# Performance work log

Measured on AMD Instinct MI355X. Metric: run time of the kernel, lower is better.

Reference implementation:

```python
import jax, jax.numpy as jnp
import numpy as np

N = 1_000_000
D_IN = 57   # hardcoded reshape(1,57) in original aggregate()
D_OUT = 128
K = 3       # num_sample=3 hardcoded in _get_unique_neighs_list


def _masked_mean_aggregate(h, neigh_idx, neigh_mask):
    # h: [N, D]; neigh_idx: [N, K] int; neigh_mask: [N, K] {0,1}
    feats = h[neigh_idx]                                   # [N, K, D] gather
    m = neigh_mask.astype(h.dtype)[..., None]              # [N, K, 1]
    s = jnp.sum(feats * m, axis=1)                         # [N, D]
    cnt = jnp.maximum(jnp.sum(neigh_mask, axis=1, keepdims=True).astype(h.dtype), 1.0)
    return s / cnt                                         # mask.mm(embed_matrix) equivalent (segment mean)


def _sage_layer(self_feats, aggregate_feats, W):
    # combined = cat([self, agg], dim=1); relu(W @ combined^T)^T; L2 normalize
    combined = jnp.concatenate([self_feats, aggregate_feats], axis=1)  # [N, 2D]
    out = jax.nn.relu(combined @ W.T)                                  # [N, out]
    norm = jnp.linalg.norm(out, axis=-1, keepdims=True)
    return out / jnp.maximum(norm, 1e-12)                              # F.normalize p=2 eps=1e-12


def setup_inputs() -> dict:
    key = jax.random.key(0)
    ks = jax.random.split(key, 7)
    x = jax.random.normal(ks[0], (N, D_IN), dtype=jnp.float32)
    W1 = jax.random.normal(ks[1], (D_OUT, 2 * D_IN), dtype=jnp.float32) * 0.1
    W2 = jax.random.normal(ks[2], (D_OUT, 2 * D_OUT), dtype=jnp.float32) * 0.1
    neigh_idx1 = jax.random.randint(ks[3], (N, K), 0, N, dtype=jnp.int32)
    neigh_mask1 = jax.random.randint(ks[4], (N, K), 0, 2, dtype=jnp.int32)
    neigh_idx2 = jax.random.randint(ks[5], (N, K), 0, N, dtype=jnp.int32)
    neigh_mask2 = jax.random.randint(ks[6], (N, K), 0, 2, dtype=jnp.int32)
    return {"x": x, "W1": W1, "W2": W2,
            "neigh_idx1": neigh_idx1, "neigh_mask1": neigh_mask1,
            "neigh_idx2": neigh_idx2, "neigh_mask2": neigh_mask2}


def reference(x, W1, W2, neigh_idx1, neigh_mask1, neigh_idx2, neigh_mask2):
    # Layer 1: aggregate over sampled neighbors of raw features, then SageLayer
    agg1 = _masked_mean_aggregate(x, neigh_idx1, neigh_mask1)
    h1 = _sage_layer(x, agg1, W1)                 # [N, D_OUT]
    # Layer 2
    agg2 = _masked_mean_aggregate(h1, neigh_idx2, neigh_mask2)
    h2 = _sage_layer(h1, agg2, W2)                # [N, D_OUT]
    return h2
```

## Files before the change

### kernel.cpp

```cpp
#include <hip/hip_runtime.h>
#include <hip/hip_bf16.h>

#define NN 1000000
#define NG 15625
#define GRID 512

typedef short bf16x8 __attribute__((ext_vector_type(8)));
typedef float f32x4  __attribute__((ext_vector_type(4)));
typedef unsigned short u16x8 __attribute__((ext_vector_type(8)));
typedef unsigned short u16x4 __attribute__((ext_vector_type(4)));

__device__ __forceinline__ float bf2f(unsigned short u){
  unsigned int x = ((unsigned int)u) << 16; float f;
  __builtin_memcpy(&f, &x, 4); return f;
}
__device__ __forceinline__ short f2bf(float v){
  __hip_bfloat16 h = __float2bfloat16(v); short s;
  __builtin_memcpy(&s, &h, 2); return s;
}

__global__ __launch_bounds__(512, 2) void sage2_mfma(
    const unsigned short* __restrict__ h1, const float* __restrict__ W2,
    const int* __restrict__ nidx, const int* __restrict__ nmask,
    float* __restrict__ out)
{
  __shared__ unsigned short comb[2][64 * 256];
  __shared__ float red[64][8];
  const int t   = threadIdx.x;
  const int l   = t & 63;
  const int w   = t >> 6;
  const int cfr = l & 15;
  const int kg  = l >> 4;

  bf16x8 Bf[8];
  #pragma unroll
  for (int ks = 0; ks < 8; ++ks) {
    const int col = w*16 + cfr;
    const int k0  = ks*32 + kg*8;
    const float* p = W2 + col*256 + k0;
    f32x4 a = *reinterpret_cast<const f32x4*>(p);
    f32x4 b = *reinterpret_cast<const f32x4*>(p + 4);
    bf16x8 v;
    v[0]=f2bf(a[0]); v[1]=f2bf(a[1]); v[2]=f2bf(a[2]); v[3]=f2bf(a[3]);
    v[4]=f2bf(b[0]); v[5]=f2bf(b[1]); v[6]=f2bf(b[2]); v[7]=f2bf(b[3]);
    Bf[ks] = v;
  }

  const u16x8* hp = reinterpret_cast<const u16x8*>(h1);

  int nib0[2], nib1[2], nib2[2], nmb0[2], nmb1[2], nmb2[2];
  u16x8 sS[2], s0[2], s1[2], s2[2];
  float m0[2], m1[2], m2[2], iv[2];

  auto IDX = [&](int g){
    const long gb = (long)g * 64;
    #pragma unroll
    for (int i = 0; i < 2; ++i) {
      int n = (t + i*512) >> 4;
      long node = gb + n;
      nib0[i] = nidx[node*3+0]; nib1[i] = nidx[node*3+1]; nib2[i] = nidx[node*3+2];
      nmb0[i] = nmask[node*3+0]; nmb1[i] = nmask[node*3+1]; nmb2[i] = nmask[node*3+2];
    }
  };
  auto GATHER = [&](int g){
    const long gb = (long)g * 64;
    #pragma unroll
    for (int i = 0; i < 2; ++i) {
      int it = t + i*512;
      int n = it >> 4, q = it & 15;
      long node = gb + n;
      int b0 = nmb0[i], b1 = nmb1[i], b2 = nmb2[i];
      m0[i]=(float)b0; m1[i]=(float)b1; m2[i]=(float)b2;
      int c = b0+b1+b2; iv[i] = 1.0f/(float)(c<1?1:c);
      u16x8 z = {};
      sS[i] = hp[node*16 + q];
      s0[i] = b0 ? hp[(long)nib0[i]*16 + q] : z;
      s1[i] = b1 ? hp[(long)nib1[i]*16 + q] : z;
      s2[i] = b2 ? hp[(long)nib2[i]*16 + q] : z;
    }
  };
  auto UNPACK = [&](int p){
    char* cb = reinterpret_cast<char*>(comb[p]);
    #pragma unroll
    for (int i = 0; i < 2; ++i) {
      int it = t + i*512;
      int n = it >> 4, q = it & 15;
      int sw = (n & 7) << 4;
      *reinterpret_cast<u16x8*>(cb + n*512 + ((q*16) ^ sw)) = sS[i];
      u16x8 r;
      #pragma unroll
      for (int j = 0; j < 8; ++j)
        r[j] = (unsigned short)f2bf(
            (m0[i]*bf2f(s0[i][j]) + m1[i]*bf2f(s1[i][j]) + m2[i]*bf2f(s2[i][j])) * iv[i]);
      *reinterpret_cast<u16x8*>(cb + n*512 + ((256 + q*16) ^ sw)) = r;
    }
  };

  const int g0 = blockIdx.x;
  IDX(g0); GATHER(g0);
  if (g0 + (int)gridDim.x < NG) IDX(g0 + gridDim.x);

  int p = 0;
  for (int g = g0; g < NG; g += gridDim.x) {
    const long gb = (long)g * 64;
    UNPACK(p);
    __syncthreads();

    int g1 = g + gridDim.x, g2 = g + 2*gridDim.x;
    if (g1 < NG) GATHER(g1);
    if (g2 < NG) IDX(g2);

    f32x4 acc[4];
    #pragma unroll
    for (int r = 0; r < 4; ++r) acc[r] = (f32x4){0.f,0.f,0.f,0.f};
    const int swz = (cfr & 7) << 4;
    char* cbp = reinterpret_cast<char*>(comb[p]);
    #pragma unroll
    for (int r = 0; r < 4; ++r) {
      const int rb = (r*16 + cfr) * 512;
      #pragma unroll
      for (int ks = 0; ks < 8; ++ks) {
        bf16x8 af = *reinterpret_cast<const bf16x8*>(cbp + rb + ((ks*64 + kg*16) ^ swz));
        acc[r] = __builtin_amdgcn_mfma_f32_16x16x32_bf16(af, Bf[ks], acc[r], 0,0,0);
      }
    }

    float ssv[4][4];
    #pragma unroll
    for (int r = 0; r < 4; ++r) {
      #pragma unroll
      for (int e = 0; e < 4; ++e) {
        float v = fmaxf(acc[r][e], 0.f); acc[r][e] = v;
        float s = v*v;
        s += __shfl_xor(s, 1); s += __shfl_xor(s, 2);
        s += __shfl_xor(s, 4); s += __shfl_xor(s, 8);
        ssv[r][e] = s;
      }
      if (cfr < 4) {
        float v = cfr==0 ? ssv[r][0] : cfr==1 ? ssv[r][1] : cfr==2 ? ssv[r][2] : ssv[r][3];
        red[r*16 + kg*4 + cfr][w] = v;
      }
    }
    __syncthreads();

    #pragma unroll
    for (int r = 0; r < 4; ++r) {
      #pragma unroll
      for (int e = 0; e < 4; ++e) {
        int row = r*16 + kg*4 + e;
        f32x4 ra = *reinterpret_cast<const f32x4*>(&red[row][0]);
        f32x4 rb = *reinterpret_cast<const f32x4*>(&red[row][4]);
        float tot = (ra[0]+ra[1]) + (ra[2]+ra[3]) + (rb[0]+rb[1]) + (rb[2]+rb[3]);
        float inv = 1.0f / fmaxf(sqrtf(tot), 1e-12f);
        out[(gb + row)*128 + w*16 + cfr] = acc[r][e] * inv;
      }
    }
    p ^= 1;
  }
}

__global__ __launch_bounds__(512, 2) void sage1_mfma(
    const float* __restrict__ x, const float* __restrict__ W1,
    const int* __restrict__ nidx, const int* __restrict__ nmask,
    unsigned short* __restrict__ h1)
{
  __shared__ unsigned short comb[2][64 * 128];
  __shared__ float red[64][8];
  const int t   = threadIdx.x;
  const int l   = t & 63;
  const int w   = t >> 6;
  const int cfr = l & 15;
  const int kg  = l >> 4;

  bf16x8 Bf[4];
  #pragma unroll
  for (int ks = 0; ks < 4; ++ks) {
    const int col = w*16 + cfr;
    const int k0  = ks*32 + kg*8;
    bf16x8 v;
    #pragma unroll
    for (int j = 0; j < 8; ++j) {
      int lk = k0 + j;
      int wk = lk < 64 ? lk : lk - 7;
      bool valid = (lk < 57) || (lk >= 64 && lk < 121);
      v[j] = valid ? f2bf(W1[col*114 + wk]) : (short)0;
    }
    Bf[ks] = v;
  }

  int nib0[2], nib1[2], nib2[2], nmb0[2], nmb1[2], nmb2[2];
  f32x4 sf[2], n0[2], n1[2], n2[2];
  float m0[2], m1[2], m2[2], iv[2];

  auto IDX = [&](int g){
    const long gb = (long)g * 64;
    #pragma unroll
    for (int i = 0; i < 2; ++i) {
      int n = (t + i*512) >> 4;
      long node = gb + n;
      nib0[i] = nidx[node*3+0]; nib1[i] = nidx[node*3+1]; nib2[i] = nidx[node*3+2];
      nmb0[i] = nmask[node*3+0]; nmb1[i] = nmask[node*3+1]; nmb2[i] = nmask[node*3+2];
    }
  };
  auto GATHER = [&](int g){
    const long gb = (long)g * 64;
    #pragma unroll
    for (int i = 0; i < 2; ++i) {
      int it = t + i*512;
      int n = it >> 4, q = it & 15;
      long node = gb + n;
      int b0 = nmb0[i], b1 = nmb1[i], b2 = nmb2[i];
      m0[i]=(float)b0; m1[i]=(float)b1; m2[i]=(float)b2;
      int c = b0+b1+b2; iv[i] = 1.0f/(float)(c<1?1:c);
      #pragma unroll
      for (int jj = 0; jj < 4; ++jj) {
        int j = q*4 + jj; int jc = j < 57 ? j : 56;
        sf[i][jj] = x[node*57 + jc];
        n0[i][jj] = b0 ? x[(long)nib0[i]*57 + jc] : 0.f;
        n1[i][jj] = b1 ? x[(long)nib1[i]*57 + jc] : 0.f;
        n2[i][jj] = b2 ? x[(long)nib2[i]*57 + jc] : 0.f;
      }
    }
  };
  auto UNPACK = [&](int p){
    char* cb = reinterpret_cast<char*>(comb[p]);
    #pragma unroll
    for (int i = 0; i < 2; ++i) {
      int it = t + i*512;
      int n = it >> 4, q = it & 15;
      int sw = (n & 7) << 4;
      u16x4 vs, va;
      #pragma unroll
      for (int jj = 0; jj < 4; ++jj) {
        vs[jj] = (unsigned short)f2bf(sf[i][jj]);
        va[jj] = (unsigned short)f2bf(
            (m0[i]*n0[i][jj] + m1[i]*n1[i][jj] + m2[i]*n2[i][jj]) * iv[i]);
      }
      *reinterpret_cast<u16x4*>(cb + n*256 + ((q*8) ^ sw))       = vs;
      *reinterpret_cast<u16x4*>(cb + n*256 + ((128 + q*8) ^ sw)) = va;
    }
  };

  const int g0 = blockIdx.x;
  IDX(g0); GATHER(g0);
  if (g0 + (int)gridDim.x < NG) IDX(g0 + gridDim.x);

  int p = 0;
  for (int g = g0; g < NG; g += gridDim.x) {
    const long gb = (long)g * 64;
    UNPACK(p);
    __syncthreads();

    int g1 = g + gridDim.x, g2 = g + 2*gridDim.x;
    if (g1 < NG) GATHER(g1);
    if (g2 < NG) IDX(g2);

    f32x4 acc[4];
    #pragma unroll
    for (int r = 0; r < 4; ++r) acc[r] = (f32x4){0.f,0.f,0.f,0.f};
    const int swz = (cfr & 7) << 4;
    char* cbp = reinterpret_cast<char*>(comb[p]);
    #pragma unroll
    for (int r = 0; r < 4; ++r) {
      const int rb = (r*16 + cfr) * 256;
      #pragma unroll
      for (int ks = 0; ks < 4; ++ks) {
        bf16x8 af = *reinterpret_cast<const bf16x8*>(cbp + rb + ((ks*64 + kg*16) ^ swz));
        acc[r] = __builtin_amdgcn_mfma_f32_16x16x32_bf16(af, Bf[ks], acc[r], 0,0,0);
      }
    }

    float ssv[4][4];
    #pragma unroll
    for (int r = 0; r < 4; ++r) {
      #pragma unroll
      for (int e = 0; e < 4; ++e) {
        float v = fmaxf(acc[r][e], 0.f); acc[r][e] = v;
        float s = v*v;
        s += __shfl_xor(s, 1); s += __shfl_xor(s, 2);
        s += __shfl_xor(s, 4); s += __shfl_xor(s, 8);
        ssv[r][e] = s;
      }
      if (cfr < 4) {
        float v = cfr==0 ? ssv[r][0] : cfr==1 ? ssv[r][1] : cfr==2 ? ssv[r][2] : ssv[r][3];
        red[r*16 + kg*4 + cfr][w] = v;
      }
    }
    __syncthreads();

    #pragma unroll
    for (int r = 0; r < 4; ++r) {
      #pragma unroll
      for (int e = 0; e < 4; ++e) {
        int row = r*16 + kg*4 + e;
        f32x4 ra = *reinterpret_cast<const f32x4*>(&red[row][0]);
        f32x4 rb = *reinterpret_cast<const f32x4*>(&red[row][4]);
        float tot = (ra[0]+ra[1]) + (ra[2]+ra[3]) + (rb[0]+rb[1]) + (rb[2]+rb[3]);
        float inv = 1.0f / fmaxf(sqrtf(tot), 1e-12f);
        h1[(gb + row)*128 + w*16 + cfr] = (unsigned short)f2bf(acc[r][e] * inv);
      }
    }
    p ^= 1;
  }
}

extern "C" void kernel_launch(void* const* d_in, const int* in_sizes, int n_in,
                              void* d_out, int out_size, void* d_ws, size_t ws_size,
                              hipStream_t stream) {
  const float* x   = (const float*)d_in[0];
  const float* W1  = (const float*)d_in[1];
  const float* W2  = (const float*)d_in[2];
  const int* idx1  = (const int*)d_in[3];
  const int* msk1  = (const int*)d_in[4];
  const int* idx2  = (const int*)d_in[5];
  const int* msk2  = (const int*)d_in[6];
  float* out = (float*)d_out;
  unsigned short* h1 = (unsigned short*)d_ws;

  sage1_mfma<<<GRID, 512, 0, stream>>>(x, W1, idx1, msk1, h1);
  sage2_mfma<<<GRID, 512, 0, stream>>>(h1, W2, idx2, msk2, out);
}
```

Measured before the change: 890.6 us.

## Restructure layer-1 kernel to 256-thread blocks with wider per-wave tiles

The layer-1 kernel moves from 512-thread blocks to 256-thread blocks with a 2048-block grid. Each wave now computes 32 output columns with two MFMA accumulators, and the double-buffered LDS is dropped for a single buffer with a simpler one-stage prefetch that fuses the index load into the gather. Columns past 57 are now zeroed instead of clamped. The layer-2 output uses nontemporal stores to avoid polluting cache. The aim is higher occupancy and fewer reduction partners, at the cost of higher register pressure and a shallower prefetch pipeline.

```diff
diff --git a/kernel.cpp b/kernel.cpp
--- a/kernel.cpp
+++ b/kernel.cpp
@@ -3,7 +3,6 @@
 
 #define NN 1000000
 #define NG 15625
-#define GRID 512
 
 typedef short bf16x8 __attribute__((ext_vector_type(8)));
 typedef float f32x4  __attribute__((ext_vector_type(4)));
@@ -36,8 +35,7 @@
   #pragma unroll
   for (int ks = 0; ks < 8; ++ks) {
     const int col = w*16 + cfr;
-    const int k0  = ks*32 + kg*8;
-    const float* p = W2 + col*256 + k0;
+    const float* p = W2 + col*256 + ks*32 + kg*8;
     f32x4 a = *reinterpret_cast<const f32x4*>(p);
     f32x4 b = *reinterpret_cast<const f32x4*>(p + 4);
     bf16x8 v;
@@ -152,81 +150,81 @@
         f32x4 rb = *reinterpret_cast<const f32x4*>(&red[row][4]);
         float tot = (ra[0]+ra[1]) + (ra[2]+ra[3]) + (rb[0]+rb[1]) + (rb[2]+rb[3]);
         float inv = 1.0f / fmaxf(sqrtf(tot), 1e-12f);
-        out[(gb + row)*128 + w*16 + cfr] = acc[r][e] * inv;
+        __builtin_nontemporal_store(acc[r][e] * inv,
+                                    &out[(gb + row)*128 + w*16 + cfr]);
       }
     }
     p ^= 1;
   }
 }
 
-__global__ __launch_bounds__(512, 2) void sage1_mfma(
+__global__ __launch_bounds__(256, 2) void sage1_mfma(
     const float* __restrict__ x, const float* __restrict__ W1,
     const int* __restrict__ nidx, const int* __restrict__ nmask,
     unsigned short* __restrict__ h1)
 {
-  __shared__ unsigned short comb[2][64 * 128];
-  __shared__ float red[64][8];
+  __shared__ unsigned short comb[64 * 128];
+  __shared__ float red[64][4];
   const int t   = threadIdx.x;
   const int l   = t & 63;
   const int w   = t >> 6;
   const int cfr = l & 15;
   const int kg  = l >> 4;
 
-  bf16x8 Bf[4];
+  bf16x8 Bf[4][2];
   #pragma unroll
   for (int ks = 0; ks < 4; ++ks) {
-    const int col = w*16 + cfr;
-    const int k0  = ks*32 + kg*8;
-    bf16x8 v;
-    #pragma unroll
-    for (int j = 0; j < 8; ++j) {
-      int lk = k0 + j;
-      int wk = lk < 64 ? lk : lk - 7;
-      bool valid = (lk < 57) || (lk >= 64 && lk < 121);
-      v[j] = valid ? f2bf(W1[col*114 + wk]) : (short)0;
-    }
-    Bf[ks] = v;
+    #pragma unroll
+    for (int nf = 0; nf < 2; ++nf) {
+      const int col = w*32 + nf*16 + cfr;
+      const int k0  = ks*32 + kg*8;
+      bf16x8 v;
+      #pragma unroll
+      for (int j = 0; j < 8; ++j) {
+        int lk = k0 + j;
+        int wk = lk < 64 ? lk : lk - 7;
+        bool valid = (lk < 57) || (lk >= 64 && lk < 121);
+        v[j] = valid ? f2bf(W1[col*114 + wk]) : (short)0;
+      }
+      Bf[ks][nf] = v;
+    }
   }
 
-  int nib0[2], nib1[2], nib2[2], nmb0[2], nmb1[2], nmb2[2];
-  f32x4 sf[2], n0[2], n1[2], n2[2];
-  float m0[2], m1[2], m2[2], iv[2];
-
-  auto IDX = [&](int g){
-    const long gb = (long)g * 64;
-    #pragma unroll
-    for (int i = 0; i < 2; ++i) {
-      int n = (t + i*512) >> 4;
-      long node = gb + n;
-      nib0[i] = nidx[node*3+0]; nib1[i] = nidx[node*3+1]; nib2[i] = nidx[node*3+2];
-      nmb0[i] = nmask[node*3+0]; nmb1[i] = nmask[node*3+1]; nmb2[i] = nmask[node*3+2];
-    }
-  };
-  auto GATHER = [&](int g){
-    const long gb = (long)g * 64;
-    #pragma unroll
-    for (int i = 0; i < 2; ++i) {
-      int it = t + i*512;
+  char* cb = reinterpret_cast<char*>(comb);
+
+  f32x4 sf[4], n0[4], n1[4], n2[4];
+  float m0[4], m1[4], m2[4], iv[4];
+
+  auto ISSUE = [&](int g){
+    const long gb = (long)g * 64;
+    #pragma unroll
+    for (int i = 0; i < 4; ++i) {
+      int it = t + i*256;
       int n = it >> 4, q = it & 15;
       long node = gb + n;
-      int b0 = nmb0[i], b1 = nmb1[i], b2 = nmb2[i];
+      int j0 = nidx[node*3+0], j1 = nidx[node*3+1], j2 = nidx[node*3+2];
+      int b0 = nmask[node*3+0], b1 = nmask[node*3+1], b2 = nmask[node*3+2];
       m0[i]=(float)b0; m1[i]=(float)b1; m2[i]=(float)b2;
       int c = b0+b1+b2; iv[i] = 1.0f/(float)(c<1?1:c);
       #pragma unroll
       for (int jj = 0; jj < 4; ++jj) {
-        int j = q*4 + jj; int jc = j < 57 ? j : 56;
-        sf[i][jj] = x[node*57 + jc];
-        n0[i][jj] = b0 ? x[(long)nib0[i]*57 + jc] : 0.f;
-        n1[i][jj] = b1 ? x[(long)nib1[i]*57 + jc] : 0.f;
-        n2[i][jj] = b2 ? x[(long)nib2[i]*57 + jc] : 0.f;
+        int j = q*4 + jj;
+        bool jv = j < 57;
+        sf[i][jj] = jv         ? x[node*57 + j]     : 0.f;
+        n0[i][jj] = (b0 && jv) ? x[(long)j0*57 + j] : 0.f;
+        n1[i][jj] = (b1 && jv) ? x[(long)j1*57 + j] : 0.f;
+        n2[i][jj] = (b2 && jv) ? x[(long)j2*57 + j] : 0.f;
       }
     }
   };
-  auto UNPACK = [&](int p){
-    char* cb = reinterpret_cast<char*>(comb[p]);
-    #pragma unroll
-    for (int i = 0; i < 2; ++i) {
-      int it = t + i*512;
+
+  if (blockIdx.x < NG) ISSUE(blockIdx.x);
+
+  for (int g = blockIdx.x; g < NG; g += gridDim.x) {
+    const long gb = (long)g * 64;
+    #pragma unroll
+    for (int i = 0; i < 4; ++i) {
+      int it = t + i*256;
       int n = it >> 4, q = it & 15;
       int sw = (n & 7) << 4;
       u16x4 vs, va;
@@ -239,34 +237,26 @@
       *reinterpret_cast<u16x4*>(cb + n*256 + ((q*8) ^ sw))       = vs;
       *reinterpret_cast<u16x4*>(cb + n*256 + ((128 + q*8) ^ sw)) = va;
     }
-  };
-
-  const int g0 = blockIdx.x;
-  IDX(g0); GATHER(g0);
-  if (g0 + (int)gridDim.x < NG) IDX(g0 + gridDim.x);
-
-  int p = 0;
-  for (int g = g0; g < NG; g += gridDim.x) {
-    const long gb = (long)g * 64;
-    UNPACK(p);
     __syncthreads();
 
-    int g1 = g + gridDim.x, g2 = g + 2*gridDim.x;
-    if (g1 < NG) GATHER(g1);
-    if (g2 < NG) IDX(g2);
-
-    f32x4 acc[4];
-    #pragma unroll
-    for (int r = 0; r < 4; ++r) acc[r] = (f32x4){0.f,0.f,0.f,0.f};
+    int gn = g + gridDim.x;
+    if (gn < NG) ISSUE(gn);
+
+    f32x4 acc[4][2];
+    #pragma unroll
+    for (int r = 0; r < 4; ++r) {
+      acc[r][0] = (f32x4){0.f,0.f,0.f,0.f};
+      acc[r][1] = (f32x4){0.f,0.f,0.f,0.f};
+    }
     const int swz = (cfr & 7) << 4;
-    char* cbp = reinterpret_cast<char*>(comb[p]);
     #pragma unroll
     for (int r = 0; r < 4; ++r) {
       const int rb = (r*16 + cfr) * 256;
       #pragma unroll
       for (int ks = 0; ks < 4; ++ks) {
-        bf16x8 af = *reinterpret_cast<const bf16x8*>(cbp + rb + ((ks*64 + kg*16) ^ swz));
-        acc[r] = __builtin_amdgcn_mfma_f32_16x16x32_bf16(af, Bf[ks], acc[r], 0,0,0);
+        bf16x8 af = *reinterpret_cast<const bf16x8*>(cb + rb + ((ks*64 + kg*16) ^ swz));
+        acc[r][0] = __builtin_amdgcn_mfma_f32_16x16x32_bf16(af, Bf[ks][0], acc[r][0], 0,0,0);
+        acc[r][1] = __builtin_amdgcn_mfma_f32_16x16x32_bf16(af, Bf[ks][1], acc[r][1], 0,0,0);
       }
     }
 
@@ -275,8 +265,9 @@
     for (int r = 0; r < 4; ++r) {
       #pragma unroll
       for (int e = 0; e < 4; ++e) {
-        float v = fmaxf(acc[r][e], 0.f); acc[r][e] = v;
-        float s = v*v;
+        float v0 = fmaxf(acc[r][0][e], 0.f); acc[r][0][e] = v0;
+        float v1 = fmaxf(acc[r][1][e], 0.f); acc[r][1][e] = v1;
+        float s = v0*v0 + v1*v1;
         s += __shfl_xor(s, 1); s += __shfl_xor(s, 2);
         s += __shfl_xor(s, 4); s += __shfl_xor(s, 8);
         ssv[r][e] = s;
@@ -293,14 +284,13 @@
       #pragma unroll
       for (int e = 0; e < 4; ++e) {
         int row = r*16 + kg*4 + e;
-        f32x4 ra = *reinterpret_cast<const f32x4*>(&red[row][0]);
-        f32x4 rb = *reinterpret_cast<const f32x4*>(&red[row][4]);
-        float tot = (ra[0]+ra[1]) + (ra[2]+ra[3]) + (rb[0]+rb[1]) + (rb[2]+rb[3]);
+        float tot = red[row][0] + red[row][1] + red[row][2] + red[row][3];
         float inv = 1.0f / fmaxf(sqrtf(tot), 1e-12f);
-        h1[(gb + row)*128 + w*16 + cfr] = (unsigned short)f2bf(acc[r][e] * inv);
-      }
-    }
-    p ^= 1;
+        long node = gb + row;
+        h1[node*128 + w*32 + cfr]      = (unsigned short)f2bf(acc[r][0][e] * inv);
+        h1[node*128 + w*32 + 16 + cfr] = (unsigned short)f2bf(acc[r][1][e] * inv);
+      }
+    }
   }
 }
 
@@ -317,6 +307,6 @@
   float* out = (float*)d_out;
   unsigned short* h1 = (unsigned short*)d_ws;
 
-  sage1_mfma<<<GRID, 512, 0, stream>>>(x, W1, idx1, msk1, h1);
-  sage2_mfma<<<GRID, 512, 0, stream>>>(h1, W2, idx2, msk2, out);
-}
+  sage1_mfma<<<2048, 256, 0, stream>>>(x, W1, idx1, msk1, h1);
+  sage2_mfma<<<512,  512, 0, stream>>>(h1, W2, idx2, msk2, out);
+}
```

Result: faster. 743.5 us (-16.5%).
